# Performance work log

Hardware: AMD Instinct MI355X
Metric: run time of the kernel (lower is better)

The kernel has to match this reference:

```python
import jax, jax.numpy as jnp
import numpy as np
from jax import lax

GROUPS = 32
CH = 2048
CG = CH // GROUPS  # 64 channels per group
H = W = 64
B = 4
EPS = 1e-5


def _conv2d(x, w, b, padding, dilation=1):
    # x: [N, Cin, H, W], w: [Cout, Cin, kh, kw] (OIHW)
    y = lax.conv_general_dilated(
        x, w, window_strides=(1, 1),
        padding=[(padding, padding), (padding, padding)],
        rhs_dilation=(dilation, dilation),
        dimension_numbers=("NCHW", "OIHW", "NCHW"))
    return y + b[None, :, None, None]


def _prelu(x, alpha):
    # single shared slope (num_parameters=1)
    return jnp.where(x >= 0, x, alpha[0] * x)


def setup_inputs() -> dict:
    key = jax.random.key(0)
    ks = jax.random.split(key, 6)
    s = 0.05
    f32 = jnp.float32
    return {
        "x": jax.random.normal(ks[0], (B, CH, H, W), f32),
        # EFFM.conv1x1 (on concatenated pooled h/w strips)
        "w_hw": jax.random.normal(ks[1], (CG, CG, 1, 1), f32) * s,
        "b_hw": jnp.zeros((CG,), f32),
        # GroupNorm(cg, cg): per-channel affine
        "gn_w": jnp.ones((CG,), f32),
        "gn_b": jnp.zeros((CG,), f32),
        # RC branch1: 3x3 conv pad=1 + PReLU
        "w_b1": jax.random.normal(ks[2], (CG, CG, 3, 3), f32) * s,
        "b_b1": jnp.zeros((CG,), f32),
        "a_b1": jnp.full((1,), 0.25, f32),
        # RC branch2: 3x3 conv dilation=2 pad=2 + PReLU
        "w_b2": jax.random.normal(ks[3], (CG, CG, 3, 3), f32) * s,
        "b_b2": jnp.zeros((CG,), f32),
        "a_b2": jnp.full((1,), 0.25, f32),
        # RC conv128to64: 1x1 conv 2*cg -> cg
        "w_cat": jax.random.normal(ks[4], (CG, 2 * CG, 1, 1), f32) * s,
        "b_cat": jnp.zeros((CG,), f32),
    }


def _effm(x, w_hw, b_hw, gn_w, gn_b, w_b1, b_b1, a_b1, w_b2, b_b2, a_b2, w_cat, b_cat):
    b, c, h, w = x.shape
    cg = c // GROUPS
    bg = b * GROUPS
    gx = x.reshape(bg, cg, h, w)

    # --- coordinate attention branch ---
    x_h = jnp.mean(gx, axis=3, keepdims=True)                       # [bg, cg, h, 1]
    x_w = jnp.mean(gx, axis=2, keepdims=True).transpose(0, 1, 3, 2)  # [bg, cg, w, 1]
    hw = jnp.concatenate([x_h, x_w], axis=2)                         # [bg, cg, h+w, 1]
    # 1x1 conv == channel mixing linear
    hw = jnp.einsum("oi,bilk->bolk", w_hw[:, :, 0, 0], hw) + b_hw[None, :, None, None]
    x_h, x_w = hw[:, :, :h, :], hw[:, :, h:, :]
    gate = gx * jax.nn.sigmoid(x_h) * jax.nn.sigmoid(x_w.transpose(0, 1, 3, 2))

    # GroupNorm(num_groups=cg, num_channels=cg) == per-channel instance norm
    mu = jnp.mean(gate, axis=(2, 3), keepdims=True)
    var = jnp.var(gate, axis=(2, 3), keepdims=True)
    x1 = (gate - mu) * lax.rsqrt(var + EPS)
    x1 = x1 * gn_w[None, :, None, None] + gn_b[None, :, None, None]

    # --- RC multi-scale branch ---
    br1 = _prelu(_conv2d(gx, w_b1, b_b1, padding=1), a_b1) + gx
    br2 = _prelu(_conv2d(gx, w_b2, b_b2, padding=2, dilation=2), a_b2) + gx
    cat = jnp.concatenate([br1, br2], axis=1)                        # [bg, 2cg, h, w]
    x2 = jnp.einsum("oi,bihw->bohw", w_cat[:, :, 0, 0], cat) + b_cat[None, :, None, None]

    # --- cross softmax-matmul attention ---
    x11 = jax.nn.softmax(jnp.mean(x1, axis=(2, 3)), axis=-1)          # [bg, cg]
    x21 = jax.nn.softmax(jnp.mean(x2, axis=(2, 3)), axis=-1)          # [bg, cg]
    weights = (jnp.einsum("gc,gchw->ghw", x11, x2)
               + jnp.einsum("gc,gchw->ghw", x21, x1))                # [bg, h, w]
    out = gx * jax.nn.sigmoid(weights)[:, None, :, :]
    return out.reshape(b, c, h, w)


def reference(x, w_hw, b_hw, gn_w, gn_b, w_b1, b_b1, a_b1, w_b2, b_b2, a_b2, w_cat, b_cat):
    return _effm(x, w_hw, b_hw, gn_w, gn_b, w_b1, b_b1, a_b1, w_b2, b_b2, a_b2, w_cat, b_cat)
```

## Files before the change

### kernel.cpp

```cpp
#include <hip/hip_runtime.h>
#include <hip/hip_bf16.h>

#define HWPX 4096

typedef __attribute__((ext_vector_type(8))) short short8v;
typedef __attribute__((ext_vector_type(4))) float f32x4;
typedef __attribute__((ext_vector_type(16))) float f32x16;
#define MFMA32(a,b,c) __builtin_amdgcn_mfma_f32_32x32x16_bf16(a,b,c,0,0,0)

__device__ __forceinline__ float sigf(float x){ return 1.0f/(1.0f+__expf(-x)); }
__device__ __forceinline__ unsigned short f2bf(float f){
  __hip_bfloat16 h = __float2bfloat16(f);
  unsigned short u; __builtin_memcpy(&u, &h, sizeof(u)); return u;
}
__device__ __forceinline__ float bf2f(unsigned short u){
  return __uint_as_float(((unsigned)u)<<16);
}
__device__ __forceinline__ void gl2lds16(const void* g, void* l){
  __builtin_amdgcn_global_load_lds((const __attribute__((address_space(1))) void*)g,
                                   (__attribute__((address_space(3))) void*)l, 16, 0, 0);
}

__global__ __launch_bounds__(256) void k_pre(const float* __restrict__ x,
                                             const float* __restrict__ wb1,
                                             const float* __restrict__ wb2,
                                             const float* __restrict__ wcat,
                                             const float* __restrict__ gnb,
                                             unsigned short* __restrict__ xb,
                                             float* __restrict__ hwbuf,
                                             unsigned short* __restrict__ wimg,
                                             unsigned short* __restrict__ wcimg,
                                             float* __restrict__ x11,
                                             float* __restrict__ x2mean){
  int bid = blockIdx.x, tid = threadIdx.x;
  if (bid >= 1088){
    int idx = (bid - 1088)*2048 + tid*8;
    f32x4 z = {0.f,0.f,0.f,0.f};
    *(f32x4*)(x2mean + idx) = z;
    *(f32x4*)(x2mean + idx + 4) = z;
    return;
  }
  if (bid >= 1024){
    int bid2 = bid - 1024;
    for (int idx = bid2*256 + tid; idx < 73728; idx += 64*256){
      int f = idx >> 9, r = idx & 511, lane = r >> 3, j = r & 7;
      int qc = f / 36, rem = f % 36, tap = rem >> 2, kc = rem & 3;
      int q = qc >> 1, conv = qc & 1, kf = kc >> 1, cot = kc & 1;
      int co = cot*32 + (lane & 31);
      int ci = q*32 + kf*16 + (lane >> 5)*8 + j;
      const float* src = conv ? wb2 : wb1;
      wimg[idx] = f2bf(src[(co*64 + ci)*9 + tap]);
    }
    if (bid2 == 0){
      for (int idx = tid; idx < 8192; idx += 256){
        int f = idx >> 9, r = idx & 511, lane = r >> 3, j = r & 7;
        int kfc = f >> 1, cot = f & 1;
        int o = cot*32 + (lane & 31);
        int ch = kfc*16 + (lane >> 5)*8 + j;
        wcimg[idx] = f2bf(wcat[o*128 + ch]);
      }
      if (tid < 64){
        float g = gnb[tid];
        float m = g;
        for (int s=32; s; s>>=1) m = fmaxf(m, __shfl_xor(m, s));
        float e = __expf(g-m);
        float se = e;
        for (int s=32; s; s>>=1) se += __shfl_xor(se, s);
        x11[tid] = e/se;
      }
    }
    return;
  }
  int g = bid >> 3, slot = bid & 7;
  int col = tid & 63, wid = tid >> 6;
  __shared__ float rsm[8*64];
  __shared__ float csm[4*8*64];
  float colacc[8] = {0,0,0,0,0,0,0,0};
  const float* xbase = x + ((size_t)(g*64 + slot*8))*HWPX;
  for (int p=0;p<16;++p){
    int r = wid + 4*p;
    const float* src = xbase + r*64 + col;
    float v[8];
    #pragma unroll
    for (int e=0;e<8;e++) v[e] = src[(size_t)e*HWPX];
    unsigned pk[4];
    #pragma unroll
    for (int j=0;j<4;j++) pk[j] = (unsigned)f2bf(v[2*j]) | ((unsigned)f2bf(v[2*j+1])<<16);
    f32x4 st; __builtin_memcpy(&st, pk, 16);
    *(f32x4*)((char*)xb + (((size_t)(g*64+r))*8 + slot)*1024 + col*16) = st;
    #pragma unroll
    for (int e=0;e<8;e++){
      float s = v[e];
      s += __shfl_xor(s,1); s += __shfl_xor(s,2); s += __shfl_xor(s,4);
      s += __shfl_xor(s,8); s += __shfl_xor(s,16); s += __shfl_xor(s,32);
      if ((tid&63)==0) rsm[e*64+r] = s;
      colacc[e] += v[e];
    }
  }
  #pragma unroll
  for (int e=0;e<8;e++) csm[(wid*8+e)*64+col] = colacc[e];
  __syncthreads();
  float* hb = hwbuf + ((size_t)(g*64 + slot*8))*128;
  for (int idx=tid; idx<512; idx+=256){
    int e = idx>>6, r = idx&63;
    hb[e*128 + r] = rsm[e*64+r] * (1.0f/64.0f);
  }
  for (int idx=tid; idx<512; idx+=256){
    int e = idx>>6, c2 = idx&63;
    float s = csm[(0*8+e)*64+c2] + csm[(1*8+e)*64+c2] + csm[(2*8+e)*64+c2] + csm[(3*8+e)*64+c2];
    hb[e*128 + 64 + c2] = s * (1.0f/64.0f);
  }
}

__global__ __launch_bounds__(256) void k_hwmm(const float* hwbuf, const float* whw,
                                              const float* bhw, float* sigbuf){
  int g = blockIdx.x;
  __shared__ float hl[64*128];
  int tid = threadIdx.x;
  const float* src = hwbuf + (size_t)g*8192;
  for (int i = tid; i < 2048; i += 256) ((float4*)hl)[i] = ((const float4*)src)[i];
  __syncthreads();
  int p  = tid & 127;
  int o0 = (tid >> 7) * 32;
  float acc[32];
  #pragma unroll
  for (int k=0;k<32;k++) acc[k] = bhw[o0+k];
  for (int i=0;i<64;i++){
    float v = hl[i*128+p];
    #pragma unroll
    for (int k=0;k<32;k++) acc[k] = fmaf(whw[(o0+k)*64+i], v, acc[k]);
  }
  float* dst = sigbuf + (size_t)g*8192;
  #pragma unroll
  for (int k=0;k<32;k++) dst[(o0+k)*128+p] = sigf(acc[k]);
}

__global__ __launch_bounds__(256) void k_gate2(const unsigned short* __restrict__ xb,
                                               const float* __restrict__ sigbuf,
                                               const float* __restrict__ gnw,
                                               const float* __restrict__ gnb,
                                               float* __restrict__ scsh){
  int bsw = blockIdx.x;
  int g = bsw >> 3, slot = bsw & 7;
  int tid = threadIdx.x, col = tid & 63, wq = tid >> 6, lane = tid & 63;
  __shared__ float srm[8*64], scm[8*64], red[4*16];
  for (int idx = tid; idx < 1024; idx += 256){
    int e = idx >> 7, k = idx & 127;
    float v = sigbuf[(size_t)g*8192 + (size_t)(slot*8+e)*128 + k];
    if (k < 64) srm[e*64+k] = v; else scm[e*64+k-64] = v;
  }
  __syncthreads();
  float s[8] = {0,0,0,0,0,0,0,0}, s2[8] = {0,0,0,0,0,0,0,0};
  const char* base = (const char*)xb + (((size_t)(g*64))*8 + slot)*1024;
  for (int p=0;p<16;++p){
    int row = wq*16 + p;
    short8v xv = *(const short8v*)(base + (size_t)row*8192 + col*16);
    #pragma unroll
    for (int e=0;e<8;e++){
      float v = bf2f((unsigned short)xv[e]) * srm[e*64+row] * scm[e*64+col];
      s[e] += v; s2[e] = fmaf(v, v, s2[e]);
    }
  }
  #pragma unroll
  for (int e=0;e<8;e++){
    #pragma unroll
    for (int off=1; off<64; off<<=1){ s[e] += __shfl_xor(s[e], off); s2[e] += __shfl_xor(s2[e], off); }
  }
  if (lane == 0){
    #pragma unroll
    for (int e=0;e<8;e++){ red[wq*16+e] = s[e]; red[wq*16+8+e] = s2[e]; }
  }
  __syncthreads();
  if (tid < 8){
    float S  = red[tid]   + red[16+tid] + red[32+tid] + red[48+tid];
    float S2 = red[8+tid] + red[24+tid] + red[40+tid] + red[56+tid];
    float mu = S*(1.f/4096.f);
    float var = S2*(1.f/4096.f) - mu*mu;
    int c = slot*8 + tid;
    float scale = rsqrtf(var + 1e-5f) * gnw[c];
    scsh[(g*64+c)*2]   = scale;
    scsh[(g*64+c)*2+1] = gnb[c] - mu*scale;
  }
}

template<int DIL>
__device__ __forceinline__ void conv_q(const char* INL, const char* WL,
                                       int ch2, int rquad, int cot, int lh, int l31, int lane,
                                       f32x16 (&acc)[4]){
  constexpr int conv = DIL - 1;
  constexpr int NROW = 4 + 2*DIL;
  #pragma unroll
  for (int kf=0; kf<2; ++kf){
    const char* ibase = INL + (kf*2 + lh)*1088 + (ch2*32 + 2 + l31)*16
                        + (rquad*4 + 2 - DIL)*4352;
    #pragma unroll
    for (int dxx=0; dxx<3; ++dxx){
      const char* ib = ibase + ((dxx-1)*DIL)*16;
      short8v Brow[NROW];
      #pragma unroll
      for (int i=0;i<NROW;++i) Brow[i] = *(const short8v*)(ib + i*4352);
      #pragma unroll
      for (int dyp=0;dyp<3;++dyp){
        int tap = dyp*3 + dxx;
        const char* wp = WL + (size_t)(((conv*9+tap)*4 + kf*2 + cot)*1024) + lane*16;
        short8v A0 = *(const short8v*)(wp);
        #pragma unroll
        for (int pt=0;pt<4;++pt)
          acc[pt] = MFMA32(A0, Brow[pt + dyp*DIL], acc[pt]);
      }
    }
  }
}

__global__ __launch_bounds__(1024) void k_convcat(const unsigned short* __restrict__ xb,
                                                  const char* __restrict__ wgl,
                                                  const char* __restrict__ wcgl,
                                                  const float* __restrict__ bb1,
                                                  const float* __restrict__ bb2,
                                                  const float* __restrict__ a1p,
                                                  const float* __restrict__ a2p,
                                                  const float* __restrict__ bcat,
                                                  const float* __restrict__ x11,
                                                  float* __restrict__ wsum2,
                                                  float* __restrict__ wsum2b,
                                                  float* __restrict__ x2mean){
  extern __shared__ char smem[];
  char* INL = smem;
  char* WL  = smem + 52224;
  char* BRL = smem;
  char* WCL = smem + 131072;
  float* x11l = (float*)(smem + 147456);
  float* bcl  = x11l + 64;

  const int tid = threadIdx.x;
  const int g = blockIdx.x >> 3;
  const int strip = blockIdx.x & 7;
  const int r0 = strip*8;
  const int w = tid >> 6;
  const int lane = tid & 63;
  const int l31 = lane & 31;
  const int lh  = lane >> 5;
  const int conv = w >> 3;
  const int ch2 = (w >> 2) & 1;
  const int rquad = (w >> 1) & 1;
  const int cot = w & 1;

  gl2lds16(wcgl + (size_t)tid*16, WCL + tid*16);
  if (tid < 64){ x11l[tid] = x11[tid]; bcl[tid] = bcat[tid]; }
  if (tid < 192){
    int seg = tid >> 2, pc = tid & 3;
    int colp = (pc < 2) ? pc : pc + 64;
    *(f32x4*)(INL + seg*1088 + colp*16) = (f32x4){0.f,0.f,0.f,0.f};
  }

  f32x16 acc[4];
  #pragma unroll
  for (int pt=0;pt<4;pt++)
    #pragma unroll
    for (int e=0;e<16;e++) acc[pt][e] = 0.f;

  for (int q=0;q<2;++q){
    if (q) __syncthreads();
    #pragma unroll
    for (int k=0;k<4;k++){
      int idx = tid + k*1024;
      gl2lds16(wgl + (size_t)q*73728 + (size_t)idx*16, WL + idx*16);
    }
    if (tid < 512){
      int idx = 4096 + tid;
      gl2lds16(wgl + (size_t)q*73728 + (size_t)idx*16, WL + idx*16);
    }
    #pragma unroll
    for (int i=0;i<3;++i){
      int seg = w*3 + i;
      int row = seg >> 2, slot = seg & 3;
      int rg = r0 - 2 + row;
      char* dst = INL + seg*1088 + 32;
      if ((unsigned)rg < 64u){
        const char* src = (const char*)xb + ((((size_t)(g*64+rg))*8) + q*4 + slot)*1024 + lane*16;
        gl2lds16(src, dst + lane*16);
      } else {
        *(f32x4*)(dst + lane*16) = (f32x4){0.f,0.f,0.f,0.f};
      }
    }
    __syncthreads();
    if (conv == 0) conv_q<1>(INL, WL, ch2, rquad, cot, lh, l31, lane, acc);
    else           conv_q<2>(INL, WL, ch2, rquad, cot, lh, l31, lane, acc);
  }
  __syncthreads();

  {
    const float alpha = conv ? a2p[0] : a1p[0];
    const float* bbp = conv ? bb2 : bb1;
    #pragma unroll
    for (int rq=0;rq<4;++rq){
      int co0 = cot*32 + 8*rq + 4*lh;
      float b0 = bbp[co0], b1 = bbp[co0+1], b2 = bbp[co0+2], b3 = bbp[co0+3];
      int ch0 = conv*64 + co0;
      #pragma unroll
      for (int pt=0;pt<4;++pt){
        int prow = rquad*4 + pt;
        int colg = ch2*32 + l31;
        const char* rsrc = (const char*)xb + (((size_t)(g*64 + r0 + prow))*8 + (co0>>3))*1024
                           + colg*16 + (co0&7)*2;
        ushort4 rv = *(const ushort4*)rsrc;
        float v0 = acc[pt][rq*4+0] + b0; v0 = (v0>=0.f? v0 : alpha*v0) + bf2f(rv.x);
        float v1 = acc[pt][rq*4+1] + b1; v1 = (v1>=0.f? v1 : alpha*v1) + bf2f(rv.y);
        float v2 = acc[pt][rq*4+2] + b2; v2 = (v2>=0.f? v2 : alpha*v2) + bf2f(rv.z);
        float v3 = acc[pt][rq*4+3] + b3; v3 = (v3>=0.f? v3 : alpha*v3) + bf2f(rv.w);
        int px = prow*64 + colg;
        int addr = (px*256 + ch0*2) ^ ((px & 15) << 4);
        ushort4 pk; pk.x=f2bf(v0); pk.y=f2bf(v1); pk.z=f2bf(v2); pk.w=f2bf(v3);
        *(ushort4*)(BRL + addr) = pk;
      }
    }
  }
  __syncthreads();

  {
    f32x16 c2[2];
    #pragma unroll
    for (int t=0;t<2;t++)
      #pragma unroll
      for (int e=0;e<16;e++) c2[t][e] = 0.f;

    #pragma unroll
    for (int kfc=0;kfc<8;++kfc){
      const char* ap = WCL + (size_t)(kfc*2 + cot)*1024 + lane*16;
      short8v A0 = *(const short8v*)(ap);
      #pragma unroll
      for (int t=0;t<2;++t){
        int px = (w>>1)*64 + t*32 + l31;
        int addr = (px*256 + kfc*32 + lh*16) ^ ((px & 15) << 4);
        short8v B = *(const short8v*)(BRL + addr);
        c2[t] = MFMA32(A0, B, c2[t]);
      }
    }
    float u0 = 0.f, u1 = 0.f;
    #pragma unroll
    for (int reg=0;reg<16;++reg){
      int o = cot*32 + (reg&3) + 8*(reg>>2) + 4*lh;
      float xw = x11l[o], bc = bcl[o];
      u0 += xw*(c2[0][reg] + bc);
      u1 += xw*(c2[1][reg] + bc);
      float sv = c2[0][reg] + c2[1][reg];
      sv += __shfl_xor(sv, 1); sv += __shfl_xor(sv, 2);
      sv += __shfl_xor(sv, 4); sv += __shfl_xor(sv, 8); sv += __shfl_xor(sv, 16);
      if (l31 == 0) atomicAdd(&x2mean[g*64 + o], sv);
    }
    u0 += __shfl_xor(u0, 32);
    u1 += __shfl_xor(u1, 32);
    if (lh == 0){
      float* wp2 = (cot ? wsum2b : wsum2) + (size_t)g*4096 + strip*512 + (w>>1)*64 + l31;
      wp2[0]  = u0;
      wp2[32] = u1;
    }
  }
}

__global__ __launch_bounds__(256) void k_final2(const unsigned short* __restrict__ xb,
                                                const float* __restrict__ sigbuf,
                                                const float* __restrict__ scsh,
                                                const float* __restrict__ x2mean,
                                                const float* __restrict__ bcat,
                                                const float* __restrict__ wsum2,
                                                const float* __restrict__ wsum2b,
                                                float* __restrict__ out){
  int blk = blockIdx.x;
  int g = blk >> 4, chunk = blk & 15;
  int tid = threadIdx.x;
  __shared__ float x21s[64];
  __shared__ float crow[64*4];
  __shared__ float ccol[64*64];
  __shared__ float Ssm;
  const float* sgb = sigbuf + (size_t)g*8192;
  if (tid < 64){
    float mean = x2mean[g*64 + tid] * (1.f/4096.f) + bcat[tid];
    float mx = mean;
    for (int s=32; s; s>>=1) mx = fmaxf(mx, __shfl_xor(mx, s));
    float e = __expf(mean - mx);
    float se = e;
    for (int s=32; s; s>>=1) se += __shfl_xor(se, s);
    x21s[tid] = e/se;
  }
  for (int idx = tid; idx < 4096; idx += 256){
    int c = idx >> 6, col = idx & 63;
    ccol[idx] = sgb[c*128 + 64 + col];
  }
  __syncthreads();
  {
    int c = tid >> 2, rr = tid & 3;
    crow[tid] = x21s[c] * scsh[(g*64+c)*2] * sgb[c*128 + chunk*4 + rr];
  }
  if (tid < 64){
    float v = x21s[tid] * scsh[(g*64+tid)*2+1];
    for (int s=32; s; s>>=1) v += __shfl_xor(v, s);
    if (tid == 0) Ssm = v;
  }
  __syncthreads();
  int px = chunk*256 + tid;
  int rr = tid >> 6, col = tid & 63;
  int row = chunk*4 + rr;
  float xv[64];
  const char* xbg = (const char*)xb + (((size_t)(g*64 + row))*8)*1024 + col*16;
  #pragma unroll
  for (int slot=0;slot<8;slot++){
    short8v v8 = *(const short8v*)(xbg + slot*1024);
    #pragma unroll
    for (int e=0;e<8;e++) xv[slot*8+e] = bf2f((unsigned short)v8[e]);
  }
  float W = wsum2[(size_t)g*4096 + px] + wsum2b[(size_t)g*4096 + px] + Ssm;
  #pragma unroll
  for (int c=0;c<64;c++){
    W = fmaf(crow[c*4+rr]*ccol[c*64+col], xv[c], W);
  }
  float s = sigf(W);
  float* op = out + (size_t)(g*64)*HWPX + px;
  #pragma unroll
  for (int c=0;c<64;c++){
    op[(size_t)c*HWPX] = xv[c] * s;
  }
}

extern "C" void kernel_launch(void* const* d_in, const int* in_sizes, int n_in,
                              void* d_out, int out_size, void* d_ws, size_t ws_size,
                              hipStream_t stream) {
  const float* x     = (const float*)d_in[0];
  const float* w_hw  = (const float*)d_in[1];
  const float* b_hw  = (const float*)d_in[2];
  const float* gn_w  = (const float*)d_in[3];
  const float* gn_b  = (const float*)d_in[4];
  const float* w_b1  = (const float*)d_in[5];
  const float* b_b1  = (const float*)d_in[6];
  const float* a_b1  = (const float*)d_in[7];
  const float* w_b2  = (const float*)d_in[8];
  const float* b_b2  = (const float*)d_in[9];
  const float* a_b2  = (const float*)d_in[10];
  const float* w_cat = (const float*)d_in[11];
  const float* b_cat = (const float*)d_in[12];

  char* ws = (char*)d_ws;
  unsigned short* wimg  = (unsigned short*)(ws + 0);
  unsigned short* wcimg = (unsigned short*)(ws + 147456);
  float* x11    = (float*)(ws + 163840);
  float* x2mean = (float*)(ws + 164096);
  float* scsh   = (float*)(ws + 196864);
  float* wsum2  = (float*)(ws + 262400);
  float* wsum2b = (float*)(ws + 2359552);
  float* hwbuf  = (float*)(ws + 4456704);
  float* sigb   = (float*)(ws + 8651008);
  unsigned short* xb = (unsigned short*)(ws + 16777216);
  float* out = (float*)d_out;

  hipFuncSetAttribute(reinterpret_cast<const void*>(k_convcat),
                      hipFuncAttributeMaxDynamicSharedMemorySize, 147968);

  k_pre  <<<1092, 256, 0, stream>>>(x, w_b1, w_b2, w_cat, gn_b, xb, hwbuf, wimg, wcimg,
                                    x11, x2mean);
  k_hwmm <<<128,  256, 0, stream>>>(hwbuf, w_hw, b_hw, sigb);
  k_gate2<<<1024, 256, 0, stream>>>(xb, sigb, gn_w, gn_b, scsh);
  k_convcat<<<1024, 1024, 147968, stream>>>(xb, (const char*)wimg, (const char*)wcimg,
                                            b_b1, b_b2, a_b1, a_b2, b_cat, x11,
                                            wsum2, wsum2b, x2mean);
  k_final2<<<2048, 256, 0, stream>>>(xb, sigb, scsh, x2mean, b_cat, wsum2, wsum2b, out);
}
```

Baseline: 269.0 us.

## Fuse GroupNorm statistics into conv epilogue and drop separate gate-stats kernel

Removes the k_gate2 kernel, which made a full extra pass over the bf16 input to compute per-channel GroupNorm sum and sum-of-squares of the gated input. Those statistics are now accumulated in the branch-1 epilogue of k_convcat, which already loads the residual input values. The partial sums are reduced with wave shuffles and combined with global atomics into zeroed buffers. k_final2 then derives scale and shift from the sums itself. This saves one kernel launch and a large memory read, at the cost of extra sigbuf loads, registers and atomics in the conv epilogue.

```diff
diff --git a/kernel.cpp b/kernel.cpp
--- a/kernel.cpp
+++ b/kernel.cpp
@@ -31,13 +31,13 @@
                                              unsigned short* __restrict__ wimg,
                                              unsigned short* __restrict__ wcimg,
                                              float* __restrict__ x11,
-                                             float* __restrict__ x2mean){
+                                             float* __restrict__ zero_base){
   int bid = blockIdx.x, tid = threadIdx.x;
   if (bid >= 1088){
     int idx = (bid - 1088)*2048 + tid*8;
     f32x4 z = {0.f,0.f,0.f,0.f};
-    *(f32x4*)(x2mean + idx) = z;
-    *(f32x4*)(x2mean + idx + 4) = z;
+    *(f32x4*)(zero_base + idx) = z;
+    *(f32x4*)(zero_base + idx + 4) = z;
     return;
   }
   if (bid >= 1024){
@@ -135,54 +135,6 @@
   for (int k=0;k<32;k++) dst[(o0+k)*128+p] = sigf(acc[k]);
 }
 
-__global__ __launch_bounds__(256) void k_gate2(const unsigned short* __restrict__ xb,
-                                               const float* __restrict__ sigbuf,
-                                               const float* __restrict__ gnw,
-                                               const float* __restrict__ gnb,
-                                               float* __restrict__ scsh){
-  int bsw = blockIdx.x;
-  int g = bsw >> 3, slot = bsw & 7;
-  int tid = threadIdx.x, col = tid & 63, wq = tid >> 6, lane = tid & 63;
-  __shared__ float srm[8*64], scm[8*64], red[4*16];
-  for (int idx = tid; idx < 1024; idx += 256){
-    int e = idx >> 7, k = idx & 127;
-    float v = sigbuf[(size_t)g*8192 + (size_t)(slot*8+e)*128 + k];
-    if (k < 64) srm[e*64+k] = v; else scm[e*64+k-64] = v;
-  }
-  __syncthreads();
-  float s[8] = {0,0,0,0,0,0,0,0}, s2[8] = {0,0,0,0,0,0,0,0};
-  const char* base = (const char*)xb + (((size_t)(g*64))*8 + slot)*1024;
-  for (int p=0;p<16;++p){
-    int row = wq*16 + p;
-    short8v xv = *(const short8v*)(base + (size_t)row*8192 + col*16);
-    #pragma unroll
-    for (int e=0;e<8;e++){
-      float v = bf2f((unsigned short)xv[e]) * srm[e*64+row] * scm[e*64+col];
-      s[e] += v; s2[e] = fmaf(v, v, s2[e]);
-    }
-  }
-  #pragma unroll
-  for (int e=0;e<8;e++){
-    #pragma unroll
-    for (int off=1; off<64; off<<=1){ s[e] += __shfl_xor(s[e], off); s2[e] += __shfl_xor(s2[e], off); }
-  }
-  if (lane == 0){
-    #pragma unroll
-    for (int e=0;e<8;e++){ red[wq*16+e] = s[e]; red[wq*16+8+e] = s2[e]; }
-  }
-  __syncthreads();
-  if (tid < 8){
-    float S  = red[tid]   + red[16+tid] + red[32+tid] + red[48+tid];
-    float S2 = red[8+tid] + red[24+tid] + red[40+tid] + red[56+tid];
-    float mu = S*(1.f/4096.f);
-    float var = S2*(1.f/4096.f) - mu*mu;
-    int c = slot*8 + tid;
-    float scale = rsqrtf(var + 1e-5f) * gnw[c];
-    scsh[(g*64+c)*2]   = scale;
-    scsh[(g*64+c)*2+1] = gnb[c] - mu*scale;
-  }
-}
-
 template<int DIL>
 __device__ __forceinline__ void conv_q(const char* INL, const char* WL,
                                        int ch2, int rquad, int cot, int lh, int l31, int lane,
@@ -215,6 +167,7 @@
 __global__ __launch_bounds__(1024) void k_convcat(const unsigned short* __restrict__ xb,
                                                   const char* __restrict__ wgl,
                                                   const char* __restrict__ wcgl,
+                                                  const float* __restrict__ sigbuf,
                                                   const float* __restrict__ bb1,
                                                   const float* __restrict__ bb2,
                                                   const float* __restrict__ a1p,
@@ -223,7 +176,9 @@
                                                   const float* __restrict__ x11,
                                                   float* __restrict__ wsum2,
                                                   float* __restrict__ wsum2b,
-                                                  float* __restrict__ x2mean){
+                                                  float* __restrict__ x2mean,
+                                                  float* __restrict__ gsum,
+                                                  float* __restrict__ gsumsq){
   extern __shared__ char smem[];
   char* INL = smem;
   char* WL  = smem + 52224;
@@ -292,26 +247,66 @@
   {
     const float alpha = conv ? a2p[0] : a1p[0];
     const float* bbp = conv ? bb2 : bb1;
+    const float* sgg = sigbuf + (size_t)g*8192;
+    const int colg = ch2*32 + l31;
+    float ssum[16], ssq[16];
+    #pragma unroll
+    for (int k=0;k<16;k++){ ssum[k]=0.f; ssq[k]=0.f; }
     #pragma unroll
     for (int rq=0;rq<4;++rq){
       int co0 = cot*32 + 8*rq + 4*lh;
       float b0 = bbp[co0], b1 = bbp[co0+1], b2 = bbp[co0+2], b3 = bbp[co0+3];
       int ch0 = conv*64 + co0;
+      float sc0=0.f, sc1=0.f, sc2=0.f, sc3=0.f;
+      if (conv == 0){
+        sc0 = sgg[(co0+0)*128 + 64 + colg];
+        sc1 = sgg[(co0+1)*128 + 64 + colg];
+        sc2 = sgg[(co0+2)*128 + 64 + colg];
+        sc3 = sgg[(co0+3)*128 + 64 + colg];
+      }
       #pragma unroll
       for (int pt=0;pt<4;++pt){
         int prow = rquad*4 + pt;
-        int colg = ch2*32 + l31;
         const char* rsrc = (const char*)xb + (((size_t)(g*64 + r0 + prow))*8 + (co0>>3))*1024
                            + colg*16 + (co0&7)*2;
         ushort4 rv = *(const ushort4*)rsrc;
-        float v0 = acc[pt][rq*4+0] + b0; v0 = (v0>=0.f? v0 : alpha*v0) + bf2f(rv.x);
-        float v1 = acc[pt][rq*4+1] + b1; v1 = (v1>=0.f? v1 : alpha*v1) + bf2f(rv.y);
-        float v2 = acc[pt][rq*4+2] + b2; v2 = (v2>=0.f? v2 : alpha*v2) + bf2f(rv.z);
-        float v3 = acc[pt][rq*4+3] + b3; v3 = (v3>=0.f? v3 : alpha*v3) + bf2f(rv.w);
+        float r0f = bf2f(rv.x), r1f = bf2f(rv.y), r2f = bf2f(rv.z), r3f = bf2f(rv.w);
+        float v0 = acc[pt][rq*4+0] + b0; v0 = (v0>=0.f? v0 : alpha*v0) + r0f;
+        float v1 = acc[pt][rq*4+1] + b1; v1 = (v1>=0.f? v1 : alpha*v1) + r1f;
+        float v2 = acc[pt][rq*4+2] + b2; v2 = (v2>=0.f? v2 : alpha*v2) + r2f;
+        float v3 = acc[pt][rq*4+3] + b3; v3 = (v3>=0.f? v3 : alpha*v3) + r3f;
         int px = prow*64 + colg;
         int addr = (px*256 + ch0*2) ^ ((px & 15) << 4);
         ushort4 pk; pk.x=f2bf(v0); pk.y=f2bf(v1); pk.z=f2bf(v2); pk.w=f2bf(v3);
         *(ushort4*)(BRL + addr) = pk;
+        if (conv == 0){
+          int rowg = r0 + prow;
+          float sr0 = sgg[(co0+0)*128 + rowg];
+          float sr1 = sgg[(co0+1)*128 + rowg];
+          float sr2 = sgg[(co0+2)*128 + rowg];
+          float sr3 = sgg[(co0+3)*128 + rowg];
+          float g0 = r0f*sr0*sc0, g1 = r1f*sr1*sc1, g2 = r2f*sr2*sc2, g3 = r3f*sr3*sc3;
+          ssum[rq*4+0] += g0; ssq[rq*4+0] = fmaf(g0,g0,ssq[rq*4+0]);
+          ssum[rq*4+1] += g1; ssq[rq*4+1] = fmaf(g1,g1,ssq[rq*4+1]);
+          ssum[rq*4+2] += g2; ssq[rq*4+2] = fmaf(g2,g2,ssq[rq*4+2]);
+          ssum[rq*4+3] += g3; ssq[rq*4+3] = fmaf(g3,g3,ssq[rq*4+3]);
+        }
+      }
+    }
+    if (conv == 0){
+      #pragma unroll
+      for (int k=0;k<16;k++){
+        float a = ssum[k], b = ssq[k];
+        a += __shfl_xor(a,1); b += __shfl_xor(b,1);
+        a += __shfl_xor(a,2); b += __shfl_xor(b,2);
+        a += __shfl_xor(a,4); b += __shfl_xor(b,4);
+        a += __shfl_xor(a,8); b += __shfl_xor(b,8);
+        a += __shfl_xor(a,16); b += __shfl_xor(b,16);
+        if (l31 == 0){
+          int o = cot*32 + 8*(k>>2) + 4*lh + (k&3);
+          atomicAdd(&gsum[g*64 + o], a);
+          atomicAdd(&gsumsq[g*64 + o], b);
+        }
       }
     }
   }
@@ -360,7 +355,10 @@
 
 __global__ __launch_bounds__(256) void k_final2(const unsigned short* __restrict__ xb,
                                                 const float* __restrict__ sigbuf,
-                                                const float* __restrict__ scsh,
+                                                const float* __restrict__ gnw,
+                                                const float* __restrict__ gnb,
+                                                const float* __restrict__ gsum,
+                                                const float* __restrict__ gsumsq,
                                                 const float* __restrict__ x2mean,
                                                 const float* __restrict__ bcat,
                                                 const float* __restrict__ wsum2,
@@ -370,6 +368,7 @@
   int g = blk >> 4, chunk = blk & 15;
   int tid = threadIdx.x;
   __shared__ float x21s[64];
+  __shared__ float scl[64], shfv[64];
   __shared__ float crow[64*4];
   __shared__ float ccol[64*64];
   __shared__ float Ssm;
@@ -382,6 +381,15 @@
     float se = e;
     for (int s=32; s; s>>=1) se += __shfl_xor(se, s);
     x21s[tid] = e/se;
+  } else if (tid < 128){
+    int c = tid - 64;
+    float S  = gsum[g*64 + c];
+    float S2 = gsumsq[g*64 + c];
+    float mu = S*(1.f/4096.f);
+    float var = S2*(1.f/4096.f) - mu*mu;
+    float sc = rsqrtf(var + 1e-5f) * gnw[c];
+    scl[c] = sc;
+    shfv[c] = gnb[c] - mu*sc;
   }
   for (int idx = tid; idx < 4096; idx += 256){
     int c = idx >> 6, col = idx & 63;
@@ -390,10 +398,10 @@
   __syncthreads();
   {
     int c = tid >> 2, rr = tid & 3;
-    crow[tid] = x21s[c] * scsh[(g*64+c)*2] * sgb[c*128 + chunk*4 + rr];
+    crow[tid] = x21s[c] * scl[c] * sgb[c*128 + chunk*4 + rr];
   }
   if (tid < 64){
-    float v = x21s[tid] * scsh[(g*64+tid)*2+1];
+    float v = x21s[tid] * shfv[tid];
     for (int s=32; s; s>>=1) v += __shfl_xor(v, s);
     if (tid == 0) Ssm = v;
   }
@@ -444,7 +452,8 @@
   unsigned short* wcimg = (unsigned short*)(ws + 147456);
   float* x11    = (float*)(ws + 163840);
   float* x2mean = (float*)(ws + 164096);
-  float* scsh   = (float*)(ws + 196864);
+  float* gsum   = (float*)(ws + 196864);
+  float* gsumsq = (float*)(ws + 229632);
   float* wsum2  = (float*)(ws + 262400);
   float* wsum2b = (float*)(ws + 2359552);
   float* hwbuf  = (float*)(ws + 4456704);
@@ -455,12 +464,12 @@
   hipFuncSetAttribute(reinterpret_cast<const void*>(k_convcat),
                       hipFuncAttributeMaxDynamicSharedMemorySize, 147968);
 
-  k_pre  <<<1092, 256, 0, stream>>>(x, w_b1, w_b2, w_cat, gn_b, xb, hwbuf, wimg, wcimg,
-                                    x11, x2mean);
+  k_pre  <<<1100, 256, 0, stream>>>(x, w_b1, w_b2, w_cat, gn_b, xb, hwbuf, wimg, wcimg,
+                                    x11, x2mean );
   k_hwmm <<<128,  256, 0, stream>>>(hwbuf, w_hw, b_hw, sigb);
-  k_gate2<<<1024, 256, 0, stream>>>(xb, sigb, gn_w, gn_b, scsh);
   k_convcat<<<1024, 1024, 147968, stream>>>(xb, (const char*)wimg, (const char*)wcimg,
-                                            b_b1, b_b2, a_b1, a_b2, b_cat, x11,
-                                            wsum2, wsum2b, x2mean);
-  k_final2<<<2048, 256, 0, stream>>>(xb, sigb, scsh, x2mean, b_cat, wsum2, wsum2b, out);
-}
+                                            sigb, b_b1, b_b2, a_b1, a_b2, b_cat, x11,
+                                            wsum2, wsum2b, x2mean, gsum, gsumsq);
+  k_final2<<<2048, 256, 0, stream>>>(xb, sigb, gn_w, gn_b, gsum, gsumsq,
+                                     x2mean, b_cat, wsum2, wsum2b, out);
+}
```

After: 324.6 us. 1.21x slower.

## Merge GroupNorm statistics kernel into conv kernel as extra blocks

Applied to the files above, without the earlier changes.

Removes the separate k_gate2 launch and runs its GroupNorm gate statistics as 256 extra 1024-thread blocks appended to k_convcat's grid, each handling four of the former 256-thread units. This saves one kernel launch and lets the memory-bound stats work overlap with the MFMA conv blocks. In exchange, the stats blocks take the convolution kernel's large dynamic LDS allocation and 1024-thread footprint, which can limit how many of them are resident at once.

```diff
diff --git a/kernel.cpp b/kernel.cpp
--- a/kernel.cpp
+++ b/kernel.cpp
@@ -135,54 +135,6 @@
   for (int k=0;k<32;k++) dst[(o0+k)*128+p] = sigf(acc[k]);
 }
 
-__global__ __launch_bounds__(256) void k_gate2(const unsigned short* __restrict__ xb,
-                                               const float* __restrict__ sigbuf,
-                                               const float* __restrict__ gnw,
-                                               const float* __restrict__ gnb,
-                                               float* __restrict__ scsh){
-  int bsw = blockIdx.x;
-  int g = bsw >> 3, slot = bsw & 7;
-  int tid = threadIdx.x, col = tid & 63, wq = tid >> 6, lane = tid & 63;
-  __shared__ float srm[8*64], scm[8*64], red[4*16];
-  for (int idx = tid; idx < 1024; idx += 256){
-    int e = idx >> 7, k = idx & 127;
-    float v = sigbuf[(size_t)g*8192 + (size_t)(slot*8+e)*128 + k];
-    if (k < 64) srm[e*64+k] = v; else scm[e*64+k-64] = v;
-  }
-  __syncthreads();
-  float s[8] = {0,0,0,0,0,0,0,0}, s2[8] = {0,0,0,0,0,0,0,0};
-  const char* base = (const char*)xb + (((size_t)(g*64))*8 + slot)*1024;
-  for (int p=0;p<16;++p){
-    int row = wq*16 + p;
-    short8v xv = *(const short8v*)(base + (size_t)row*8192 + col*16);
-    #pragma unroll
-    for (int e=0;e<8;e++){
-      float v = bf2f((unsigned short)xv[e]) * srm[e*64+row] * scm[e*64+col];
-      s[e] += v; s2[e] = fmaf(v, v, s2[e]);
-    }
-  }
-  #pragma unroll
-  for (int e=0;e<8;e++){
-    #pragma unroll
-    for (int off=1; off<64; off<<=1){ s[e] += __shfl_xor(s[e], off); s2[e] += __shfl_xor(s2[e], off); }
-  }
-  if (lane == 0){
-    #pragma unroll
-    for (int e=0;e<8;e++){ red[wq*16+e] = s[e]; red[wq*16+8+e] = s2[e]; }
-  }
-  __syncthreads();
-  if (tid < 8){
-    float S  = red[tid]   + red[16+tid] + red[32+tid] + red[48+tid];
-    float S2 = red[8+tid] + red[24+tid] + red[40+tid] + red[56+tid];
-    float mu = S*(1.f/4096.f);
-    float var = S2*(1.f/4096.f) - mu*mu;
-    int c = slot*8 + tid;
-    float scale = rsqrtf(var + 1e-5f) * gnw[c];
-    scsh[(g*64+c)*2]   = scale;
-    scsh[(g*64+c)*2+1] = gnb[c] - mu*scale;
-  }
-}
-
 template<int DIL>
 __device__ __forceinline__ void conv_q(const char* INL, const char* WL,
                                        int ch2, int rquad, int cot, int lh, int l31, int lane,
@@ -215,6 +167,9 @@
 __global__ __launch_bounds__(1024) void k_convcat(const unsigned short* __restrict__ xb,
                                                   const char* __restrict__ wgl,
                                                   const char* __restrict__ wcgl,
+                                                  const float* __restrict__ sigbuf,
+                                                  const float* __restrict__ gnw,
+                                                  const float* __restrict__ gnb,
                                                   const float* __restrict__ bb1,
                                                   const float* __restrict__ bb2,
                                                   const float* __restrict__ a1p,
@@ -223,8 +178,60 @@
                                                   const float* __restrict__ x11,
                                                   float* __restrict__ wsum2,
                                                   float* __restrict__ wsum2b,
-                                                  float* __restrict__ x2mean){
+                                                  float* __restrict__ x2mean,
+                                                  float* __restrict__ scsh){
   extern __shared__ char smem[];
+  const int tid = threadIdx.x;
+
+  if (blockIdx.x >= 1024){
+    int grp = tid >> 8;
+    int tl  = tid & 255;
+    int unit = (blockIdx.x - 1024)*4 + grp;
+    int g = unit >> 3, slot = unit & 7;
+    int col = tl & 63, wq = tl >> 6, lane = tl & 63;
+    float* srm = (float*)smem + grp*1088;
+    float* scm = srm + 512;
+    float* red = scm + 512;
+    for (int idx = tl; idx < 1024; idx += 256){
+      int e = idx >> 7, k = idx & 127;
+      float v = sigbuf[(size_t)g*8192 + (size_t)(slot*8+e)*128 + k];
+      if (k < 64) srm[e*64+k] = v; else scm[e*64+k-64] = v;
+    }
+    __syncthreads();
+    float s[8] = {0,0,0,0,0,0,0,0}, s2[8] = {0,0,0,0,0,0,0,0};
+    const char* base = (const char*)xb + (((size_t)(g*64))*8 + slot)*1024;
+    for (int p=0;p<16;++p){
+      int row = wq*16 + p;
+      short8v xv = *(const short8v*)(base + (size_t)row*8192 + col*16);
+      #pragma unroll
+      for (int e=0;e<8;e++){
+        float v = bf2f((unsigned short)xv[e]) * srm[e*64+row] * scm[e*64+col];
+        s[e] += v; s2[e] = fmaf(v, v, s2[e]);
+      }
+    }
+    #pragma unroll
+    for (int e=0;e<8;e++){
+      #pragma unroll
+      for (int off=1; off<64; off<<=1){ s[e] += __shfl_xor(s[e], off); s2[e] += __shfl_xor(s2[e], off); }
+    }
+    if (lane == 0){
+      #pragma unroll
+      for (int e=0;e<8;e++){ red[wq*16+e] = s[e]; red[wq*16+8+e] = s2[e]; }
+    }
+    __syncthreads();
+    if (tl < 8){
+      float S  = red[tl]   + red[16+tl] + red[32+tl] + red[48+tl];
+      float S2 = red[8+tl] + red[24+tl] + red[40+tl] + red[56+tl];
+      float mu = S*(1.f/4096.f);
+      float var = S2*(1.f/4096.f) - mu*mu;
+      int c = slot*8 + tl;
+      float scale = rsqrtf(var + 1e-5f) * gnw[c];
+      scsh[(g*64+c)*2]   = scale;
+      scsh[(g*64+c)*2+1] = gnb[c] - mu*scale;
+    }
+    return;
+  }
+
   char* INL = smem;
   char* WL  = smem + 52224;
   char* BRL = smem;
@@ -232,7 +239,6 @@
   float* x11l = (float*)(smem + 147456);
   float* bcl  = x11l + 64;
 
-  const int tid = threadIdx.x;
   const int g = blockIdx.x >> 3;
   const int strip = blockIdx.x & 7;
   const int r0 = strip*8;
@@ -458,9 +464,8 @@
   k_pre  <<<1092, 256, 0, stream>>>(x, w_b1, w_b2, w_cat, gn_b, xb, hwbuf, wimg, wcimg,
                                     x11, x2mean);
   k_hwmm <<<128,  256, 0, stream>>>(hwbuf, w_hw, b_hw, sigb);
-  k_gate2<<<1024, 256, 0, stream>>>(xb, sigb, gn_w, gn_b, scsh);
-  k_convcat<<<1024, 1024, 147968, stream>>>(xb, (const char*)wimg, (const char*)wcimg,
-                                            b_b1, b_b2, a_b1, a_b2, b_cat, x11,
-                                            wsum2, wsum2b, x2mean);
+  k_convcat<<<1280, 1024, 147968, stream>>>(xb, (const char*)wimg, (const char*)wcimg,
+                                            sigb, gn_w, gn_b, b_b1, b_b2, a_b1, a_b2,
+                                            b_cat, x11, wsum2, wsum2b, x2mean, scsh);
   k_final2<<<2048, 256, 0, stream>>>(xb, sigb, scsh, x2mean, b_cat, wsum2, wsum2b, out);
 }
```

After: 264.4 us, median of 2. No clear change (-1.7%).
